# Kernel tuning notes

Hardware: AMD Instinct MI355X
Metric: run time of the kernel (lower is better)

## Reference

```python
import jax, jax.numpy as jnp
import numpy as np

B, S, D, H = 4, 1024, 1024, 16
HD = D // H
EPS = 1e-5


def layer_norm(x, scale, shift):
    mean = jnp.mean(x, axis=-1, keepdims=True)
    var = jnp.mean((x - mean) ** 2, axis=-1, keepdims=True)
    return scale * (x - mean) / jnp.sqrt(var + EPS) + shift


def gelu_tanh(x):
    c = jnp.sqrt(jnp.asarray(2.0 / jnp.pi, dtype=x.dtype))
    return 0.5 * x * (1.0 + jnp.tanh(c * (x + 0.044715 * x ** 3)))


def setup_inputs() -> dict:
    key = jax.random.key(0)
    ks = jax.random.split(key, 12)
    s = 0.02
    return {
        "x": jax.random.normal(ks[0], (B, S, D), dtype=jnp.float32),
        "attention_mask": jnp.ones((B, S), dtype=jnp.int32),
        "wq": jax.random.normal(ks[1], (D, D), dtype=jnp.float32) * s,
        "wk": jax.random.normal(ks[2], (D, D), dtype=jnp.float32) * s,
        "wv": jax.random.normal(ks[3], (D, D), dtype=jnp.float32) * s,
        "wo": jax.random.normal(ks[4], (D, D), dtype=jnp.float32) * s,
        "bo": jnp.zeros((D,), dtype=jnp.float32),
        "ln1_scale": jnp.ones((D,), dtype=jnp.float32),
        "ln1_shift": jnp.zeros((D,), dtype=jnp.float32),
        "ln2_scale": jnp.ones((D,), dtype=jnp.float32),
        "ln2_shift": jnp.zeros((D,), dtype=jnp.float32),
        "w1": jax.random.normal(ks[5], (D, 4 * D), dtype=jnp.float32) * s,
        "b1": jnp.zeros((4 * D,), dtype=jnp.float32),
        "w2": jax.random.normal(ks[6], (4 * D, D), dtype=jnp.float32) * s,
        "b2": jnp.zeros((D,), dtype=jnp.float32),
    }


def reference(x, attention_mask, wq, wk, wv, wo, bo, ln1_scale, ln1_shift,
              ln2_scale, ln2_shift, w1, b1, w2, b2):
    b, s, d = x.shape
    # --- pre-norm attention ---
    shortcut = x
    h = layer_norm(x, ln1_scale, ln1_shift)
    q = (h @ wq).reshape(b, s, H, HD).transpose(0, 2, 1, 3)  # bhsd
    k = (h @ wk).reshape(b, s, H, HD).transpose(0, 2, 1, 3)
    v = (h @ wv).reshape(b, s, H, HD).transpose(0, 2, 1, 3)
    scores = jnp.einsum('bhqd,bhkd->bhqk', q, k)
    causal = jnp.triu(jnp.ones((s, s), dtype=bool), k=1)  # True above diag -> masked
    neg_inf = jnp.asarray(-jnp.inf, dtype=scores.dtype)
    scores = jnp.where(causal, neg_inf, scores)
    pad = attention_mask[:, None, None, :].astype(bool)  # (b,1,1,k)
    scores = jnp.where(pad, scores, neg_inf)
    attn = jax.nn.softmax(scores / jnp.sqrt(jnp.asarray(HD, dtype=scores.dtype)), axis=-1)
    ctx = jnp.einsum('bhqk,bhkd->bhqd', attn, v)
    ctx = ctx.transpose(0, 2, 1, 3).reshape(b, s, d)
    x = shortcut + (ctx @ wo + bo)
    # --- pre-norm FFN ---
    shortcut = x
    h = layer_norm(x, ln2_scale, ln2_shift)
    h = gelu_tanh(h @ w1 + b1) @ w2 + b2
    return shortcut + h
```

## Files before the change

kernel.cpp:

```cpp
#include <hip/hip_runtime.h>
#include <hip/hip_bf16.h>
#include <math.h>

#define B_ 4
#define S_ 1024
#define D_ 1024
#define H_ 16
#define HD_ 64

typedef __hip_bfloat16 bf16_t;
typedef __attribute__((ext_vector_type(8))) short bf16x8;
typedef __attribute__((ext_vector_type(4))) float floatx4;

__device__ __forceinline__ float bf2f(ushort u) {
  return __uint_as_float((unsigned)u << 16);
}

__global__ __launch_bounds__(256) void prep_kernel(
    const float* __restrict__ x, const float* __restrict__ ln1s,
    const float* __restrict__ ln1b, bf16_t* __restrict__ h,
    const float* __restrict__ wq, const float* __restrict__ wk,
    const float* __restrict__ wv, const float* __restrict__ wo,
    const float* __restrict__ w1, const float* __restrict__ w2,
    bf16_t* __restrict__ wqkv_t, bf16_t* __restrict__ wo_t,
    bf16_t* __restrict__ w1_t, bf16_t* __restrict__ w2_t) {
  const int id = blockIdx.x;
  if (id < 4096) {
    const int row = id;
    float4 v = ((const float4*)(x + (size_t)row * D_))[threadIdx.x];
    float s = v.x + v.y + v.z + v.w;
    float ss = v.x * v.x + v.y * v.y + v.z * v.z + v.w * v.w;
#pragma unroll
    for (int off = 32; off > 0; off >>= 1) {
      s += __shfl_xor(s, off);
      ss += __shfl_xor(ss, off);
    }
    __shared__ float ls[4], lss[4], stats[2];
    const int wave = threadIdx.x >> 6, lane = threadIdx.x & 63;
    if (lane == 0) { ls[wave] = s; lss[wave] = ss; }
    __syncthreads();
    if (threadIdx.x == 0) {
      float t = ls[0] + ls[1] + ls[2] + ls[3];
      float tt = lss[0] + lss[1] + lss[2] + lss[3];
      float mean = t * (1.0f / D_);
      stats[0] = mean;
      stats[1] = rsqrtf(tt * (1.0f / D_) - mean * mean + 1e-5f);
    }
    __syncthreads();
    const float mean = stats[0], rstd = stats[1];
    float4 sc = ((const float4*)ln1s)[threadIdx.x];
    float4 sh = ((const float4*)ln1b)[threadIdx.x];
    bf16_t ob[4];
    ob[0] = __float2bfloat16(sc.x * (v.x - mean) * rstd + sh.x);
    ob[1] = __float2bfloat16(sc.y * (v.y - mean) * rstd + sh.y);
    ob[2] = __float2bfloat16(sc.z * (v.z - mean) * rstd + sh.z);
    ob[3] = __float2bfloat16(sc.w * (v.w - mean) * rstd + sh.w);
    *(ushort4*)(h + (size_t)row * D_ + threadIdx.x * 4) = *(ushort4*)ob;
    return;
  }
  const float* W;
  bf16_t* Wt;
  int K, N, n0, k0;
  if (id < 8192) {
    const int t = id - 4096, which = t >> 10, tile = t & 1023;
    n0 = (tile & 31) * 32;
    k0 = (tile >> 5) * 32;
    K = 1024; N = 1024;
    W = which == 0 ? wq : which == 1 ? wk : which == 2 ? wv : wo;
    Wt = which < 3 ? wqkv_t + (size_t)which * 1024 * 1024 : wo_t;
  } else if (id < 12288) {
    const int tile = id - 8192;
    n0 = (tile & 127) * 32;
    k0 = (tile >> 7) * 32;
    K = 1024; N = 4096;
    W = w1; Wt = w1_t;
  } else {
    const int tile = id - 12288;
    n0 = (tile & 31) * 32;
    k0 = (tile >> 5) * 32;
    K = 4096; N = 1024;
    W = w2; Wt = w2_t;
  }
  __shared__ float t[32][33];
  const int lx = threadIdx.x & 31, ly = threadIdx.x >> 5;
#pragma unroll
  for (int r = ly; r < 32; r += 8) t[r][lx] = W[(size_t)(k0 + r) * N + n0 + lx];
  __syncthreads();
#pragma unroll
  for (int r = ly; r < 32; r += 8)
    Wt[(size_t)(n0 + r) * K + k0 + lx] = __float2bfloat16(t[lx][r]);
}

__global__ __launch_bounds__(256) void mgemm_kernel(const bf16_t* __restrict__ A,
                                                    const bf16_t* __restrict__ Bt,
                                                    const float* __restrict__ bias,
                                                    void* __restrict__ C,
                                                    int M, int N, int K, int Kc,
                                                    int Mt, int Nt, int PM,
                                                    int mode) {
  __shared__ bf16_t As[128 * 64];
  __shared__ bf16_t Bs[128 * 64];
  const int tid = threadIdx.x;
  const int lane = tid & 63, w = tid >> 6;

  const int flat = blockIdx.x;
  const int xcd = flat & 7;
  int t0 = flat >> 3;
  const int mb = xcd % PM, nb = xcd / PM;
  const int mt = mb * Mt + (t0 % Mt);
  t0 /= Mt;
  const int nt = nb * Nt + (t0 % Nt);
  const int z = t0 / Nt;
  const int m0 = mt * 128, n0 = nt * 128;
  const int kz0 = z * Kc;
  const int wm = (w >> 1) * 64, wn = (w & 1) * 64;

  floatx4 zero = {0.f, 0.f, 0.f, 0.f};
  floatx4 acc[4][4];
#pragma unroll
  for (int i = 0; i < 4; i++)
#pragma unroll
    for (int j = 0; j < 4; j++) acc[i][j] = zero;

  const int ro8 = lane >> 3;
  const int g8 = ((lane & 7) ^ ro8) * 8;
  const bf16_t* ga[4];
  const bf16_t* gb[4];
  bf16_t* la[4];
  bf16_t* lb[4];
#pragma unroll
  for (int t = 0; t < 4; t++) {
    const int c = w + 4 * t;
    ga[t] = A + (size_t)(m0 + c * 8 + ro8) * K + g8;
    gb[t] = Bt + (size_t)(n0 + c * 8 + ro8) * K + g8;
    la[t] = &As[c * 512];
    lb[t] = &Bs[c * 512];
  }

  const int fr = lane & 15, quad = lane >> 4;

  for (int k0 = kz0; k0 < kz0 + Kc; k0 += 64) {
    __syncthreads();
#pragma unroll
    for (int t = 0; t < 4; t++) {
      __builtin_amdgcn_global_load_lds(
          (const __attribute__((address_space(1))) void*)(ga[t] + k0),
          (__attribute__((address_space(3))) void*)la[t], 16, 0, 0);
      __builtin_amdgcn_global_load_lds(
          (const __attribute__((address_space(1))) void*)(gb[t] + k0),
          (__attribute__((address_space(3))) void*)lb[t], 16, 0, 0);
    }
    __syncthreads();

#pragma unroll
    for (int ks = 0; ks < 2; ks++) {
      const int sq = ((quad + 4 * ks) ^ (fr & 7)) * 8;
      bf16x8 af[4], bfr[4];
#pragma unroll
      for (int i = 0; i < 4; i++) {
        af[i] = *(const bf16x8*)&As[(wm + i * 16 + fr) * 64 + sq];
        bfr[i] = *(const bf16x8*)&Bs[(wn + i * 16 + fr) * 64 + sq];
      }
#pragma unroll
      for (int i = 0; i < 4; i++)
#pragma unroll
        for (int j = 0; j < 4; j++)
          acc[i][j] = __builtin_amdgcn_mfma_f32_16x16x32_bf16(af[i], bfr[j],
                                                              acc[i][j], 0, 0, 0);
    }
  }

  bf16_t* Pz = (mode == 4) ? ((bf16_t*)C + (size_t)z * M * N) : nullptr;
#pragma unroll
  for (int j = 0; j < 4; j++) {
    const int col = n0 + wn + j * 16 + fr;
    const float bj = bias ? bias[col] : 0.f;
#pragma unroll
    for (int i = 0; i < 4; i++) {
      const int rbase = m0 + wm + i * 16 + quad * 4;
#pragma unroll
      for (int r = 0; r < 4; r++) {
        const int row = rbase + r;
        float c = acc[i][j][r] + bj;
        if (mode == 1) {
          const float xg = c;
          const float t = 0.7978845608028654f * (xg + 0.044715f * xg * xg * xg);
          const float th = 2.0f / (1.0f + __expf(-2.0f * t)) - 1.0f;
          c = 0.5f * xg * (1.0f + th);
        }
        if (mode == 4) {
          Pz[(size_t)row * N + col] = __float2bfloat16(c);
        } else {
          ((bf16_t*)C)[(size_t)row * N + col] = __float2bfloat16(c);
        }
      }
    }
  }
}

__global__ __launch_bounds__(512, 2) void mgemm256_kernel(
    const bf16_t* __restrict__ A, const bf16_t* __restrict__ Bt,
    const float* __restrict__ bias, void* __restrict__ C, int M, int N, int K,
    int Kc, int Mt, int Nt, int PM, int mode) {
  __shared__ bf16_t sm[2][2][256 * 64];
  const int tid = threadIdx.x;
  const int lane = tid & 63, w = tid >> 6;

  const int flat = blockIdx.x;
  const int xcd = flat & 7;
  int t0 = flat >> 3;
  const int mb = xcd % PM, nb = xcd / PM;
  const int mt = mb * Mt + (t0 % Mt);
  t0 /= Mt;
  const int nt = nb * Nt + (t0 % Nt);
  const int z = t0 / Nt;
  const int m0 = mt * 256, n0 = nt * 256;
  const int kz0 = z * Kc;
  const int wr = w >> 2, wc = w & 3;

  floatx4 zero = {0.f, 0.f, 0.f, 0.f};
  floatx4 acc[8][4];
#pragma unroll
  for (int i = 0; i < 8; i++)
#pragma unroll
    for (int j = 0; j < 4; j++) acc[i][j] = zero;

  const int ro8 = lane >> 3;
  const int g8 = ((lane & 7) ^ ro8) * 8;
  const bf16_t* gAb = A + (size_t)(m0 + w * 8 + ro8) * K + g8;
  const bf16_t* gBb = Bt + (size_t)(n0 + w * 8 + ro8) * K + g8;
  const size_t cstride = (size_t)64 * K;

  auto STAGE = [&](int bufi, int kk) {
#pragma unroll
    for (int tt = 0; tt < 4; ++tt) {
      __builtin_amdgcn_global_load_lds(
          (const __attribute__((address_space(1))) void*)(gAb + kk +
                                                          (size_t)tt * cstride),
          (__attribute__((address_space(3))) void*)&sm[bufi][0][w * 512 +
                                                                tt * 4096],
          16, 0, 0);
      __builtin_amdgcn_global_load_lds(
          (const __attribute__((address_space(1))) void*)(gBb + kk +
                                                          (size_t)tt * cstride),
          (__attribute__((address_space(3))) void*)&sm[bufi][1][w * 512 +
                                                                tt * 4096],
          16, 0, 0);
    }
  };

  const int fr = lane & 15, quad = lane >> 4;
  const int ntk = Kc >> 6;

  STAGE(0, kz0);
  if (ntk > 1) STAGE(1, kz0 + 64);

  for (int t = 0; t < ntk; ++t) {
    if (t + 1 < ntk) {
      asm volatile("s_waitcnt vmcnt(8)" ::: "memory");
    } else {
      asm volatile("s_waitcnt vmcnt(0)" ::: "memory");
    }
    __builtin_amdgcn_s_barrier();
    const int bi = t & 1;
#pragma unroll
    for (int ks = 0; ks < 2; ks++) {
      const int sq = ((quad + 4 * ks) ^ (fr & 7)) * 8;
      bf16x8 bfr[4];
#pragma unroll
      for (int j = 0; j < 4; j++)
        bfr[j] = *(const bf16x8*)&sm[bi][1][(wc * 64 + j * 16 + fr) * 64 + sq];
#pragma unroll
      for (int mi = 0; mi < 2; mi++) {
        bf16x8 af[4];
#pragma unroll
        for (int i = 0; i < 4; i++)
          af[i] = *(const bf16x8*)&sm[bi][0]
                      [(wr * 128 + mi * 64 + i * 16 + fr) * 64 + sq];
#pragma unroll
        for (int i = 0; i < 4; i++)
#pragma unroll
          for (int j = 0; j < 4; j++)
            acc[mi * 4 + i][j] = __builtin_amdgcn_mfma_f32_16x16x32_bf16(
                af[i], bfr[j], acc[mi * 4 + i][j], 0, 0, 0);
      }
    }
    asm volatile("s_waitcnt lgkmcnt(0)" ::: "memory");
    __builtin_amdgcn_sched_barrier(0);
    __builtin_amdgcn_s_barrier();
    if (t + 2 < ntk) STAGE(bi, kz0 + (t + 2) * 64);
  }

  bf16_t* Pz = (mode == 4) ? ((bf16_t*)C + (size_t)z * M * N) : (bf16_t*)C;
#pragma unroll
  for (int j = 0; j < 4; j++) {
    const int col = n0 + wc * 64 + j * 16 + fr;
    const float bj = bias ? bias[col] : 0.f;
#pragma unroll
    for (int i = 0; i < 8; i++) {
      const int rbase = m0 + wr * 128 + i * 16 + quad * 4;
#pragma unroll
      for (int r = 0; r < 4; r++) {
        float c = acc[i][j][r] + bj;
        if (mode == 1) {
          const float xg = c;
          const float t2 = 0.7978845608028654f * (xg + 0.044715f * xg * xg * xg);
          const float th = 2.0f / (1.0f + __expf(-2.0f * t2)) - 1.0f;
          c = 0.5f * xg * (1.0f + th);
        }
        Pz[(size_t)(rbase + r) * N + col] = __float2bfloat16(c);
      }
    }
  }
}

__global__ __launch_bounds__(256) void reduce2_ln_kernel(
    const bf16_t* __restrict__ P, size_t slice, const float* __restrict__ x,
    const float* __restrict__ bias, const float* __restrict__ scale,
    const float* __restrict__ shift, float* __restrict__ out,
    bf16_t* __restrict__ h) {
  const int row = blockIdx.x;
  const size_t e = (size_t)row * D_ + threadIdx.x * 4;
  const float4 xv = *(const float4*)(x + e);
  const ushort4 p0 = *(const ushort4*)((const ushort*)P + e);
  const ushort4 p1 = *(const ushort4*)((const ushort*)P + slice + e);
  const float4 bb = *(const float4*)(bias + threadIdx.x * 4);
  float4 v;
  v.x = xv.x + bf2f(p0.x) + bf2f(p1.x) + bb.x;
  v.y = xv.y + bf2f(p0.y) + bf2f(p1.y) + bb.y;
  v.z = xv.z + bf2f(p0.z) + bf2f(p1.z) + bb.z;
  v.w = xv.w + bf2f(p0.w) + bf2f(p1.w) + bb.w;
  *(float4*)(out + e) = v;

  float s = v.x + v.y + v.z + v.w;
  float ss = v.x * v.x + v.y * v.y + v.z * v.z + v.w * v.w;
#pragma unroll
  for (int off = 32; off > 0; off >>= 1) {
    s += __shfl_xor(s, off);
    ss += __shfl_xor(ss, off);
  }
  __shared__ float ls[4], lss[4], stats[2];
  const int wave = threadIdx.x >> 6, lane = threadIdx.x & 63;
  if (lane == 0) { ls[wave] = s; lss[wave] = ss; }
  __syncthreads();
  if (threadIdx.x == 0) {
    float t = ls[0] + ls[1] + ls[2] + ls[3];
    float tt = lss[0] + lss[1] + lss[2] + lss[3];
    float mean = t * (1.0f / D_);
    stats[0] = mean;
    stats[1] = rsqrtf(tt * (1.0f / D_) - mean * mean + 1e-5f);
  }
  __syncthreads();
  const float mean = stats[0], rstd = stats[1];
  const float4 sc = *(const float4*)(scale + threadIdx.x * 4);
  const float4 sh = *(const float4*)(shift + threadIdx.x * 4);
  bf16_t ob[4];
  ob[0] = __float2bfloat16(sc.x * (v.x - mean) * rstd + sh.x);
  ob[1] = __float2bfloat16(sc.y * (v.y - mean) * rstd + sh.y);
  ob[2] = __float2bfloat16(sc.z * (v.z - mean) * rstd + sh.z);
  ob[3] = __float2bfloat16(sc.w * (v.w - mean) * rstd + sh.w);
  *(ushort4*)(h + e) = *(ushort4*)ob;
}

__global__ __launch_bounds__(256) void reduce4_kernel(const bf16_t* __restrict__ P,
                                                      size_t slice,
                                                      const float* __restrict__ bias,
                                                      float* __restrict__ out,
                                                      int N) {
  const size_t e = ((size_t)blockIdx.x * 256 + threadIdx.x) * 4;
  const ushort* Pu = (const ushort*)P;
  const ushort4 p0 = *(const ushort4*)(Pu + e);
  const ushort4 p1 = *(const ushort4*)(Pu + slice + e);
  const ushort4 p2 = *(const ushort4*)(Pu + 2 * slice + e);
  const ushort4 p3 = *(const ushort4*)(Pu + 3 * slice + e);
  const float4 r = *(const float4*)(out + e);
  const float4 bb = *(const float4*)(bias + (int)(e % N));
  float4 o;
  o.x = r.x + bb.x + bf2f(p0.x) + bf2f(p1.x) + bf2f(p2.x) + bf2f(p3.x);
  o.y = r.y + bb.y + bf2f(p0.y) + bf2f(p1.y) + bf2f(p2.y) + bf2f(p3.y);
  o.z = r.z + bb.z + bf2f(p0.z) + bf2f(p1.z) + bf2f(p2.z) + bf2f(p3.z);
  o.w = r.w + bb.w + bf2f(p0.w) + bf2f(p1.w) + bf2f(p2.w) + bf2f(p3.w);
  *(float4*)(out + e) = o;
}

__global__ __launch_bounds__(256) void fattn_kernel(const bf16_t* __restrict__ QK,
                                                    const bf16_t* __restrict__ VT,
                                                    const int* __restrict__ mask,
                                                    bf16_t* __restrict__ O) {
  const int qt = gridDim.x - 1 - blockIdx.x;
  const int h = blockIdx.y, b = blockIdx.z;
  const int tid = threadIdx.x;
  const int lane = tid & 63, w = tid >> 6;
  const int tx = lane & 15, quad = lane >> 4;
  const int q0 = qt * 64;

  __shared__ bf16_t Ks[64 * 64];
  __shared__ bf16_t Vs[64 * 64];
  __shared__ ushort Ps[64 * 64];

  const int ro8 = lane >> 3;
  const int g8 = ((lane & 7) ^ ro8) * 8;
  const bf16_t* gk[2];
  const bf16_t* gv[2];
  bf16_t* lk[2];
  bf16_t* lv[2];
#pragma unroll
  for (int t = 0; t < 2; t++) {
    const int c = w + 4 * t;
    gk[t] = QK + (size_t)((size_t)b * S_ + c * 8 + ro8) * 2048 + 1024 + h * HD_ + g8;
    gv[t] = VT + (size_t)(h * HD_ + c * 8 + ro8) * 4096 + (size_t)b * S_ + g8;
    lk[t] = &Ks[c * 512];
    lv[t] = &Vs[c * 512];
  }

  bf16x8 qf[2];
#pragma unroll
  for (int ks = 0; ks < 2; ks++)
    qf[ks] = *(const bf16x8*)(QK + (size_t)((size_t)b * S_ + q0 + w * 16 + tx) * 2048 +
                              h * HD_ + ks * 32 + quad * 8);

  const short oneb = 0x3F80;
  bf16x8 vones = {oneb, oneb, oneb, oneb, oneb, oneb, oneb, oneb};

  floatx4 ctx[4], lacc;
#pragma unroll
  for (int nt = 0; nt < 4; nt++) {
    ctx[nt].x = 0.f; ctx[nt].y = 0.f; ctx[nt].z = 0.f; ctx[nt].w = 0.f;
  }
  lacc.x = 0.f; lacc.y = 0.f; lacc.z = 0.f; lacc.w = 0.f;

  for (int kt = 0; kt <= qt; kt++) {
    const int k0 = kt * 64;
    __syncthreads();
#pragma unroll
    for (int t = 0; t < 2; t++) {
      __builtin_amdgcn_global_load_lds(
          (const __attribute__((address_space(1))) void*)(gk[t] + (size_t)k0 * 2048),
          (__attribute__((address_space(3))) void*)lk[t], 16, 0, 0);
      __builtin_amdgcn_global_load_lds(
          (const __attribute__((address_space(1))) void*)(gv[t] + k0),
          (__attribute__((address_space(3))) void*)lv[t], 16, 0, 0);
    }
    __syncthreads();

    floatx4 accS[4];
#pragma unroll
    for (int nt = 0; nt < 4; nt++) {
      accS[nt].x = 0.f; accS[nt].y = 0.f; accS[nt].z = 0.f; accS[nt].w = 0.f;
    }
#pragma unroll
    for (int ks = 0; ks < 2; ks++) {
      const int sq = ((quad + 4 * ks) ^ (tx & 7)) * 8;
      bf16x8 kf[4];
#pragma unroll
      for (int nt = 0; nt < 4; nt++)
        kf[nt] = *(const bf16x8*)&Ks[(nt * 16 + tx) * 64 + sq];
#pragma unroll
      for (int nt = 0; nt < 4; nt++)
        accS[nt] = __builtin_amdgcn_mfma_f32_16x16x32_bf16(qf[ks], kf[nt],
                                                           accS[nt], 0, 0, 0);
    }

#pragma unroll
    for (int nt = 0; nt < 4; nt++) {
      const int jc = k0 + nt * 16 + tx;
      const bool ok = mask[b * S_ + jc] != 0;
      const int col = nt * 16 + tx;
#pragma unroll
      for (int r = 0; r < 4; r++) {
        const int qq = quad * 4 + r;
        const int qrow = q0 + w * 16 + qq;
        float p = exp2f(accS[nt][r] * 0.1803368801111244f);
        if (jc > qrow || !ok) p = 0.f;
        const int pc = ((((col >> 3) ^ (qq & 7)) << 3)) | (col & 7);
        Ps[(w * 16 + qq) * 64 + pc] =
            ((__hip_bfloat16_raw)__float2bfloat16(p)).x;
      }
    }

#pragma unroll
    for (int ks = 0; ks < 2; ks++) {
      const int sq = ((quad + 4 * ks) ^ (tx & 7)) * 8;
      const bf16x8 pf = *(const bf16x8*)&Ps[(w * 16 + tx) * 64 + sq];
      bf16x8 vf[4];
#pragma unroll
      for (int nt = 0; nt < 4; nt++)
        vf[nt] = *(const bf16x8*)&Vs[(nt * 16 + tx) * 64 + sq];
#pragma unroll
      for (int nt = 0; nt < 4; nt++)
        ctx[nt] = __builtin_amdgcn_mfma_f32_16x16x32_bf16(pf, vf[nt],
                                                          ctx[nt], 0, 0, 0);
      lacc = __builtin_amdgcn_mfma_f32_16x16x32_bf16(pf, vones, lacc, 0, 0, 0);
    }
  }

  const size_t obase = (size_t)b * S_ * D_ + (size_t)h * HD_;
  float rinv[4];
#pragma unroll
  for (int r = 0; r < 4; r++) rinv[r] = 1.0f / lacc[r];
#pragma unroll
  for (int nt = 0; nt < 4; nt++)
#pragma unroll
    for (int r = 0; r < 4; r++) {
      const int q = q0 + w * 16 + quad * 4 + r;
      O[obase + (size_t)q * D_ + nt * 16 + tx] =
          __float2bfloat16(ctx[nt][r] * rinv[r]);
    }
}

extern "C" void kernel_launch(void* const* d_in, const int* in_sizes, int n_in,
                              void* d_out, int out_size, void* d_ws, size_t ws_size,
                              hipStream_t stream) {
  const float* x = (const float*)d_in[0];
  const int* mask = (const int*)d_in[1];
  const float* wq = (const float*)d_in[2];
  const float* wk = (const float*)d_in[3];
  const float* wv = (const float*)d_in[4];
  const float* wo = (const float*)d_in[5];
  const float* bo = (const float*)d_in[6];
  const float* ln2s = (const float*)d_in[9];
  const float* ln2b = (const float*)d_in[10];
  const float* w1 = (const float*)d_in[11];
  const float* b1 = (const float*)d_in[12];
  const float* w2 = (const float*)d_in[13];
  const float* b2 = (const float*)d_in[14];
  float* out = (float*)d_out;

  const int M = B_ * S_;
  char* ws = (char*)d_ws;
  const size_t MB = (size_t)1 << 20;
  bf16_t* qk = (bf16_t*)(ws);
  bf16_t* vT = (bf16_t*)(ws + 16 * MB);
  bf16_t* ffn1 = (bf16_t*)(ws);
  bf16_t* ctx = (bf16_t*)(ws + 32 * MB);
  bf16_t* h = (bf16_t*)(ws + 40 * MB);
  bf16_t* wqkv_t = (bf16_t*)(ws + 48 * MB);
  bf16_t* wo_t = (bf16_t*)(ws + 54 * MB);
  bf16_t* w1_t = (bf16_t*)(ws + 56 * MB);
  bf16_t* w2_t = (bf16_t*)(ws + 64 * MB);
  bf16_t* Pa = (bf16_t*)(ws);
  bf16_t* Pf = (bf16_t*)(ws + 32 * MB);
  const size_t slice = (size_t)M * D_;

  prep_kernel<<<dim3(16384), 256, 0, stream>>>(x, (const float*)d_in[7],
                                               (const float*)d_in[8], h, wq, wk,
                                               wv, wo, w1, w2, wqkv_t, wo_t,
                                               w1_t, w2_t);

  mgemm_kernel<<<dim3(16 * 32), 256, 0, stream>>>(
      h, wqkv_t, nullptr, qk, M, 2 * D_, D_, D_, 8, 8, 4, 0);

  mgemm_kernel<<<dim3(8 * 32), 256, 0, stream>>>(
      wqkv_t + (size_t)2 * 1024 * 1024, h, nullptr, vT, D_, M, D_, D_,
      4, 8, 2, 0);

  fattn_kernel<<<dim3(S_ / 64, H_, B_), 256, 0, stream>>>(qk, vT, mask, ctx);

  mgemm_kernel<<<dim3(8 * 32 * 2), 256, 0, stream>>>(
      ctx, wo_t, nullptr, Pa, M, D_, D_, D_ / 2, 4, 8, 8, 4);

  reduce2_ln_kernel<<<dim3(M), 256, 0, stream>>>(Pa, slice, x, bo, ln2s, ln2b,
                                                 out, h);

  mgemm256_kernel<<<dim3(256), 512, 0, stream>>>(
      h, w1_t, b1, ffn1, M, 4 * D_, D_, D_, 4, 8, 4, 1);

  mgemm256_kernel<<<dim3(256), 512, 0, stream>>>(
      ffn1, w2_t, nullptr, Pf, M, D_, 4 * D_, D_, 2, 4, 8, 4);

  reduce4_kernel<<<dim3((size_t)M * D_ / 1024), 256, 0, stream>>>(
      Pf, slice, b2, out, D_);
}
```

Baseline: 348.8 us.

## Restructure 256x256 GEMM mainloop into quarter-phases with interleaved prefetch and LDS-staged epilogue

The 256-tile GEMM main loop is split into four sub-phases per K-step. Each phase loads fragments from LDS and issues the next K-step's global-to-LDS prefetch early, then runs MFMAs at raised priority. This replaces the old wait-all-then-compute double-buffer scheme and is meant to overlap memory traffic with matrix math. The epilogue now stages bf16 results through swizzled LDS so each row is written with 16-byte vector stores instead of scattered 2-byte writes. The cost is more barriers per K-step, and the loop now prefetches only one step ahead.

New measurement: 354.1 us. Within noise of the previous version (+1.5%).

```diff
diff --git a/kernel.cpp b/kernel.cpp
--- a/kernel.cpp
+++ b/kernel.cpp
@@ -202,7 +202,7 @@
     const bf16_t* __restrict__ A, const bf16_t* __restrict__ Bt,
     const float* __restrict__ bias, void* __restrict__ C, int M, int N, int K,
     int Kc, int Mt, int Nt, int PM, int mode) {
-  __shared__ bf16_t sm[2][2][256 * 64];
+  __shared__ bf16_t sm[65536];
   const int tid = threadIdx.x;
   const int lane = tid & 63, w = tid >> 6;
 
@@ -227,24 +227,18 @@
 
   const int ro8 = lane >> 3;
   const int g8 = ((lane & 7) ^ ro8) * 8;
-  const bf16_t* gAb = A + (size_t)(m0 + w * 8 + ro8) * K + g8;
-  const bf16_t* gBb = Bt + (size_t)(n0 + w * 8 + ro8) * K + g8;
-  const size_t cstride = (size_t)64 * K;
-
-  auto STAGE = [&](int bufi, int kk) {
-#pragma unroll
-    for (int tt = 0; tt < 4; ++tt) {
+  const bf16_t* gA0 = A + (size_t)(m0 + w * 8 + ro8) * K + g8;
+  const bf16_t* gB0 = Bt + (size_t)(n0 + w * 8 + ro8) * K + g8;
+
+  auto STAGE = [&](int bufi, int mat, int half, int kk) {
+    const bf16_t* g0 = (mat == 0) ? gA0 : gB0;
+#pragma unroll
+    for (int l = 0; l < 2; ++l) {
+      const bf16_t* src = g0 + (size_t)(half * 128 + l * 64) * K + kk;
       __builtin_amdgcn_global_load_lds(
-          (const __attribute__((address_space(1))) void*)(gAb + kk +
-                                                          (size_t)tt * cstride),
-          (__attribute__((address_space(3))) void*)&sm[bufi][0][w * 512 +
-                                                                tt * 4096],
-          16, 0, 0);
-      __builtin_amdgcn_global_load_lds(
-          (const __attribute__((address_space(1))) void*)(gBb + kk +
-                                                          (size_t)tt * cstride),
-          (__attribute__((address_space(3))) void*)&sm[bufi][1][w * 512 +
-                                                                tt * 4096],
+          (const __attribute__((address_space(1))) void*)src,
+          (__attribute__((address_space(3))) void*)
+              &sm[((bufi * 2 + mat) * 2 + half) * 8192 + (l * 8 + w) * 512],
           16, 0, 0);
     }
   };
@@ -252,65 +246,84 @@
   const int fr = lane & 15, quad = lane >> 4;
   const int ntk = Kc >> 6;
 
-  STAGE(0, kz0);
-  if (ntk > 1) STAGE(1, kz0 + 64);
+  STAGE(0, 0, 0, kz0); STAGE(0, 0, 1, kz0);
+  STAGE(0, 1, 0, kz0); STAGE(0, 1, 1, kz0);
+  asm volatile("s_waitcnt vmcnt(0)" ::: "memory");
+  __builtin_amdgcn_s_barrier();
 
   for (int t = 0; t < ntk; ++t) {
-    if (t + 1 < ntk) {
-      asm volatile("s_waitcnt vmcnt(8)" ::: "memory");
-    } else {
-      asm volatile("s_waitcnt vmcnt(0)" ::: "memory");
-    }
-    __builtin_amdgcn_s_barrier();
-    const int bi = t & 1;
-#pragma unroll
-    for (int ks = 0; ks < 2; ks++) {
-      const int sq = ((quad + 4 * ks) ^ (fr & 7)) * 8;
-      bf16x8 bfr[4];
-#pragma unroll
-      for (int j = 0; j < 4; j++)
-        bfr[j] = *(const bf16x8*)&sm[bi][1][(wc * 64 + j * 16 + fr) * 64 + sq];
-#pragma unroll
-      for (int mi = 0; mi < 2; mi++) {
-        bf16x8 af[4];
-#pragma unroll
-        for (int i = 0; i < 4; i++)
-          af[i] = *(const bf16x8*)&sm[bi][0]
-                      [(wr * 128 + mi * 64 + i * 16 + fr) * 64 + sq];
-#pragma unroll
-        for (int i = 0; i < 4; i++)
-#pragma unroll
-          for (int j = 0; j < 4; j++)
-            acc[mi * 4 + i][j] = __builtin_amdgcn_mfma_f32_16x16x32_bf16(
-                af[i], bfr[j], acc[mi * 4 + i][j], 0, 0, 0);
+    const int buf = t & 1, nbuf = buf ^ 1;
+    const int kn = kz0 + (t + 1) * 64;
+    const bool pre = (t + 1 < ntk);
+#pragma unroll
+    for (int p = 0; p < 4; ++p) {
+      const int mh = p >> 1, jh = p & 1;
+      bf16x8 af[2][4], bfr[2][2];
+#pragma unroll
+      for (int ks = 0; ks < 2; ++ks) {
+        const int sq = ((quad + 4 * ks) ^ (fr & 7)) * 8;
+#pragma unroll
+        for (int i = 0; i < 4; ++i)
+          af[ks][i] = *(const bf16x8*)&sm[((buf * 2 + 0) * 2 + wr) * 8192 +
+                                          ((mh * 4 + i) * 16 + fr) * 64 + sq];
+#pragma unroll
+        for (int j = 0; j < 2; ++j)
+          bfr[ks][j] =
+              *(const bf16x8*)&sm[((buf * 2 + 1) * 2 + (wc >> 1)) * 8192 +
+                                  ((wc & 1) * 64 + (jh * 2 + j) * 16 + fr) * 64 +
+                                  sq];
       }
-    }
-    asm volatile("s_waitcnt lgkmcnt(0)" ::: "memory");
-    __builtin_amdgcn_sched_barrier(0);
-    __builtin_amdgcn_s_barrier();
-    if (t + 2 < ntk) STAGE(bi, kz0 + (t + 2) * 64);
-  }
-
+      if (p == 0 && pre) { STAGE(nbuf, 0, 0, kn); STAGE(nbuf, 0, 1, kn); }
+      if (p == 1 && pre) { STAGE(nbuf, 1, 0, kn); STAGE(nbuf, 1, 1, kn); }
+      asm volatile("s_waitcnt lgkmcnt(8)" ::: "memory");
+      __builtin_amdgcn_s_barrier();
+      asm volatile("s_waitcnt lgkmcnt(0)" ::: "memory");
+      __builtin_amdgcn_sched_barrier(0);
+      __builtin_amdgcn_s_setprio(1);
+#pragma unroll
+      for (int ks = 0; ks < 2; ++ks)
+#pragma unroll
+        for (int i = 0; i < 4; ++i)
+#pragma unroll
+          for (int j = 0; j < 2; ++j)
+            acc[mh * 4 + i][jh * 2 + j] = __builtin_amdgcn_mfma_f32_16x16x32_bf16(
+                af[ks][i], bfr[ks][j], acc[mh * 4 + i][jh * 2 + j], 0, 0, 0);
+      __builtin_amdgcn_s_setprio(0);
+      if (p == 3) asm volatile("s_waitcnt vmcnt(0)" ::: "memory");
+      __builtin_amdgcn_s_barrier();
+    }
+  }
+
+  __syncthreads();
+  bf16_t* sl = sm + w * 8192;
   bf16_t* Pz = (mode == 4) ? ((bf16_t*)C + (size_t)z * M * N) : (bf16_t*)C;
-#pragma unroll
-  for (int j = 0; j < 4; j++) {
-    const int col = n0 + wc * 64 + j * 16 + fr;
-    const float bj = bias ? bias[col] : 0.f;
-#pragma unroll
-    for (int i = 0; i < 8; i++) {
-      const int rbase = m0 + wr * 128 + i * 16 + quad * 4;
-#pragma unroll
-      for (int r = 0; r < 4; r++) {
-        float c = acc[i][j][r] + bj;
+  float bj[4];
+#pragma unroll
+  for (int j = 0; j < 4; ++j)
+    bj[j] = bias ? bias[n0 + wc * 64 + j * 16 + fr] : 0.f;
+#pragma unroll
+  for (int i = 0; i < 8; ++i)
+#pragma unroll
+    for (int j = 0; j < 4; ++j)
+#pragma unroll
+      for (int r = 0; r < 4; ++r) {
+        const int row = i * 16 + quad * 4 + r, col = j * 16 + fr;
+        float c = acc[i][j][r] + bj[j];
         if (mode == 1) {
           const float xg = c;
           const float t2 = 0.7978845608028654f * (xg + 0.044715f * xg * xg * xg);
           const float th = 2.0f / (1.0f + __expf(-2.0f * t2)) - 1.0f;
           c = 0.5f * xg * (1.0f + th);
         }
-        Pz[(size_t)(rbase + r) * N + col] = __float2bfloat16(c);
+        const int cg = (col >> 3) ^ (row & 7);
+        sl[row * 64 + cg * 8 + (col & 7)] = __float2bfloat16(c);
       }
-    }
+#pragma unroll
+  for (int it = 0; it < 16; ++it) {
+    const int gi = it * 64 + lane;
+    const int row = gi >> 3, g = gi & 7;
+    const bf16x8 vv = *(const bf16x8*)&sl[row * 64 + ((g ^ (row & 7)) * 8)];
+    *(bf16x8*)&Pz[(size_t)(m0 + wr * 128 + row) * N + n0 + wc * 64 + g * 8] = vv;
   }
 }
 
```
